# Performance work log

Hardware: AMD Instinct MI355X
Metric: run time of the kernel (lower is better)

The kernel has to match this reference:

```python
import jax, jax.numpy as jnp
import numpy as np

N_NODES = 50000
N_EDGES = 1200000
NODE_DIM = 64
HIDDEN = 64
OUT_DIM = 1
N_LAYERS = 3


def setup_inputs() -> dict:
    key = jax.random.key(0)
    ks = jax.random.split(key, 16)
    inp = {
        "H": jax.random.normal(ks[0], (N_NODES, NODE_DIM), dtype=jnp.float32),
        "edge_index": jax.random.randint(ks[1], (2, N_EDGES), 0, N_NODES, dtype=jnp.int64),
        "E": jax.random.normal(ks[2], (N_EDGES, 16), dtype=jnp.float32),
    }
    # per-layer params: node_encoder (enc) and update_w (upd); weights stored [in, out]
    for i in range(N_LAYERS):
        in_dim = NODE_DIM if i == 0 else HIDDEN
        s = 1.0 / np.sqrt(in_dim)
        inp[f"enc_w{i}"] = jax.random.uniform(ks[3 + 2 * i], (in_dim, HIDDEN), jnp.float32, -s, s)
        inp[f"enc_b{i}"] = jax.random.uniform(ks[4 + 2 * i], (HIDDEN,), jnp.float32, -s, s)
        sh = 1.0 / np.sqrt(HIDDEN)
        inp[f"upd_w{i}"] = jax.random.uniform(ks[9 + 2 * i], (HIDDEN, HIDDEN), jnp.float32, -sh, sh)
        inp[f"upd_b{i}"] = jax.random.uniform(ks[10 + 2 * i], (HIDDEN,), jnp.float32, -sh, sh)
    so = 1.0 / np.sqrt(HIDDEN)
    inp["out_w"] = jax.random.uniform(ks[15], (HIDDEN, OUT_DIM), jnp.float32, -so, so)
    inp["out_b"] = jnp.zeros((OUT_DIM,), jnp.float32)
    return inp


def _gcn_forward(H, edge_index, params):
    u, v = edge_index[0], edge_index[1]
    # symmetric normalization with implicit self-loop degree bump (calc_norm_factor)
    deg = jax.ops.segment_sum(jnp.ones(u.shape[0], H.dtype), u, num_segments=N_NODES) + 1.0
    dis = deg ** -0.5  # deg >= 1, never inf
    norm = dis[u] * dis[v]  # [n_edges]
    for i in range(N_LAYERS):
        enc_w, enc_b, upd_w, upd_b = params[i]
        H = H @ enc_w + enc_b                      # node_encoder
        msgs = norm[:, None] * H[u]                # gather + scale
        agg = jax.ops.segment_sum(msgs, v, num_segments=N_NODES)  # scatter-add
        H = jax.nn.relu((agg + H) @ upd_w + upd_b)  # update + ReLU (dropout = identity in eval)
    return H


def reference(H, edge_index, E, enc_w0, enc_b0, upd_w0, upd_b0, enc_w1, enc_b1,
              upd_w1, upd_b1, enc_w2, enc_b2, upd_w2, upd_b2, out_w, out_b):
    params = [(enc_w0, enc_b0, upd_w0, upd_b0),
              (enc_w1, enc_b1, upd_w1, upd_b1),
              (enc_w2, enc_b2, upd_w2, upd_b2)]
    Hf = _gcn_forward(H, edge_index, params)
    graph_emb = jnp.mean(Hf, axis=0, keepdims=True)  # [1, HIDDEN] readout (batch=None)
    return graph_emb @ out_w + out_b                 # [1, OUT_DIM]
```

## Files before the change

kernel.cpp:

```cpp
#include <hip/hip_runtime.h>
#include <hip/hip_fp16.h>

#define NN 50000
#define NE 1200000
#define DIM 64
#define NB 782
#define SLICES 512
#define ES 2344
#define VCAP 2048
#define GB 782
#define FRONT_LDS 33792


__device__ __forceinline__ void lsort_body(char* smem, const int* __restrict__ ei,
                                           ushort* __restrict__ usort,
                                           int* __restrict__ ebuf,
                                           int* __restrict__ lpart_u,
                                           int* __restrict__ lpart_v,
                                           int s) {
    int* hist = (int*)smem;
    int* wsum = (int*)(smem + 3136);
    ushort* sbu = (ushort*)(smem + 4160);
    int* sbv = (int*)(smem + 8848);
    int t = threadIdx.x;
    int w = t >> 6, l = t & 63;
    int e0 = s * ES, e1 = min(e0 + ES, NE), len = e1 - e0;
    int i0 = t * 4;

    for (int i = t; i < NB; i += 256) hist[i] = 0;
    __syncthreads();
    for (int e = e0 + t; e < e1; e += 256) atomicAdd(&hist[ei[e] >> 6], 1);
    __syncthreads();
    {
        int h0 = (i0 + 0 < NB) ? hist[i0 + 0] : 0;
        int h1 = (i0 + 1 < NB) ? hist[i0 + 1] : 0;
        int h2 = (i0 + 2 < NB) ? hist[i0 + 2] : 0;
        int h3 = (i0 + 3 < NB) ? hist[i0 + 3] : 0;
        int p1 = h0, p2 = h0 + h1, p3 = p2 + h2, p4 = p3 + h3;
        int inc = p4;
        for (int o = 1; o < 64; o <<= 1) {
            int x = __shfl_up(inc, o, 64);
            if (l >= o) inc += x;
        }
        if (l == 63) wsum[w] = inc;
        __syncthreads();
        int base = 0;
#pragma unroll
        for (int j = 0; j < 4; ++j) if (j < w) base += wsum[j];
        int total = wsum[0] + wsum[1] + wsum[2] + wsum[3];
        int excl = base + inc - p4;
        int* lpu = lpart_u + s * (NB + 1);
        if (i0 + 0 < NB) { lpu[i0 + 0] = excl;      hist[i0 + 0] = excl; }
        if (i0 + 1 < NB) { lpu[i0 + 1] = excl + p1; hist[i0 + 1] = excl + p1; }
        if (i0 + 2 < NB) { lpu[i0 + 2] = excl + p2; hist[i0 + 2] = excl + p2; }
        if (i0 + 3 < NB) { lpu[i0 + 3] = excl + p3; hist[i0 + 3] = excl + p3; }
        if (t == 255) lpu[NB] = total;
    }
    __syncthreads();
    for (int e = e0 + t; e < e1; e += 256) {
        int u = ei[e];
        int pos = atomicAdd(&hist[u >> 6], 1);
        sbu[pos] = (ushort)u;
    }
    __syncthreads();
    for (int i = t; i < len; i += 256) usort[e0 + i] = sbu[i];
    for (int i = t; i < NB; i += 256) hist[i] = 0;
    __syncthreads();

    for (int e = e0 + t; e < e1; e += 256) atomicAdd(&hist[ei[NE + e] >> 6], 1);
    __syncthreads();
    {
        int h0 = (i0 + 0 < NB) ? hist[i0 + 0] : 0;
        int h1 = (i0 + 1 < NB) ? hist[i0 + 1] : 0;
        int h2 = (i0 + 2 < NB) ? hist[i0 + 2] : 0;
        int h3 = (i0 + 3 < NB) ? hist[i0 + 3] : 0;
        int p1 = h0, p2 = h0 + h1, p3 = p2 + h2, p4 = p3 + h3;
        int inc = p4;
        for (int o = 1; o < 64; o <<= 1) {
            int x = __shfl_up(inc, o, 64);
            if (l >= o) inc += x;
        }
        if (l == 63) wsum[w] = inc;
        __syncthreads();
        int base = 0;
#pragma unroll
        for (int j = 0; j < 4; ++j) if (j < w) base += wsum[j];
        int total = wsum[0] + wsum[1] + wsum[2] + wsum[3];
        int excl = base + inc - p4;
        int* lpv = lpart_v + s * (NB + 1);
        if (i0 + 0 < NB) { lpv[i0 + 0] = excl;      hist[i0 + 0] = excl; }
        if (i0 + 1 < NB) { lpv[i0 + 1] = excl + p1; hist[i0 + 1] = excl + p1; }
        if (i0 + 2 < NB) { lpv[i0 + 2] = excl + p2; hist[i0 + 2] = excl + p2; }
        if (i0 + 3 < NB) { lpv[i0 + 3] = excl + p3; hist[i0 + 3] = excl + p3; }
        if (t == 255) lpv[NB] = total;
    }
    __syncthreads();
    for (int e = e0 + t; e < e1; e += 256) {
        int u = ei[e], v = ei[NE + e];
        int pos = atomicAdd(&hist[v >> 6], 1);
        sbv[pos] = u | ((v & 63) << 16);
    }
    __syncthreads();
    for (int i = t; i < len; i += 256) ebuf[e0 + i] = sbv[i];
}

__device__ __forceinline__ void gemm_h_body(char* smem, int blk,
                                            const float* __restrict__ A,
                                            const float* __restrict__ W,
                                            const float* __restrict__ bias,
                                            __half* __restrict__ Ch, int M) {
    float (*As)[68] = (float(*)[68])smem;
    float (*Bs)[64] = (float(*)[64])(smem + 17408);
    int t = threadIdx.x;
    int row0 = blk * 64;
#pragma unroll
    for (int i = 0; i < 4; ++i) {
        int idx = t + i * 256;
        int r = idx >> 4, c = (idx & 15) << 2;
        float4 val = make_float4(0.f, 0.f, 0.f, 0.f);
        if (row0 + r < M) val = *(const float4*)&A[(size_t)(row0 + r) * DIM + c];
        *(float4*)&As[r][c] = val;
        *(float4*)&Bs[r][c] = *(const float4*)&W[r * DIM + c];
    }
    __syncthreads();
    int r0 = (t >> 4) * 4;
    int c0 = (t & 15) * 4;
    float acc[4][4] = {};
#pragma unroll
    for (int k = 0; k < 64; k += 4) {
        float4 b0 = *(float4*)&Bs[k + 0][c0];
        float4 b1 = *(float4*)&Bs[k + 1][c0];
        float4 b2 = *(float4*)&Bs[k + 2][c0];
        float4 b3 = *(float4*)&Bs[k + 3][c0];
#pragma unroll
        for (int i = 0; i < 4; ++i) {
            float4 av = *(float4*)&As[r0 + i][k];
            acc[i][0] = fmaf(av.x, b0.x, fmaf(av.y, b1.x, fmaf(av.z, b2.x, fmaf(av.w, b3.x, acc[i][0]))));
            acc[i][1] = fmaf(av.x, b0.y, fmaf(av.y, b1.y, fmaf(av.z, b2.y, fmaf(av.w, b3.y, acc[i][1]))));
            acc[i][2] = fmaf(av.x, b0.z, fmaf(av.y, b1.z, fmaf(av.z, b2.z, fmaf(av.w, b3.z, acc[i][2]))));
            acc[i][3] = fmaf(av.x, b0.w, fmaf(av.y, b1.w, fmaf(av.z, b2.w, fmaf(av.w, b3.w, acc[i][3]))));
        }
    }
    float4 bv = *(const float4*)&bias[c0];
#pragma unroll
    for (int i = 0; i < 4; ++i) {
        int r = row0 + r0 + i;
        if (r < M) {
            __half2 p0 = __floats2half2_rn(acc[i][0] + bv.x, acc[i][1] + bv.y);
            __half2 p1 = __floats2half2_rn(acc[i][2] + bv.z, acc[i][3] + bv.w);
            uint2 pk;
            pk.x = *(unsigned int*)&p0;
            pk.y = *(unsigned int*)&p1;
            *(uint2*)&Ch[(size_t)r * DIM + c0] = pk;
        }
    }
}

__global__ __launch_bounds__(256) void k_front(const int* __restrict__ ei,
                                               ushort* __restrict__ usort,
                                               int* __restrict__ ebuf,
                                               int* __restrict__ lpart_u,
                                               int* __restrict__ lpart_v,
                                               const float* __restrict__ A,
                                               const float* __restrict__ W,
                                               const float* __restrict__ bias,
                                               __half* __restrict__ Ch) {
    extern __shared__ char smem[];
    int b = blockIdx.x;
    if (b < 256)
        lsort_body(smem, ei, usort, ebuf, lpart_u, lpart_v, b);
    else if (b < 512)
        gemm_h_body(smem, b - 256, A, W, bias, Ch, NN);
    else if (b < 768)
        lsort_body(smem, ei, usort, ebuf, lpart_u, lpart_v, b - 256);
    else
        gemm_h_body(smem, b - 512, A, W, bias, Ch, NN);
}

__global__ __launch_bounds__(256) void k_mid(const ushort* __restrict__ usort,
                                             const int* __restrict__ lpart_u,
                                             float* __restrict__ dis,
                                             float* __restrict__ colsum) {
    __shared__ int sh[64];
    int b = blockIdx.x;
    int t = threadIdx.x;
    if (b == 0 && t < 64) colsum[t] = 0.f;
    if (t < 64) sh[t] = 0;
    __syncthreads();
    for (int s = t; s < SLICES; s += 256) {
        const int* row = lpart_u + s * (NB + 1);
        int st = row[b], en = row[b + 1];
        for (int i = st; i < en; ++i)
            atomicAdd(&sh[usort[s * ES + i] & 63], 1);
    }
    __syncthreads();
    int n = (b << 6) + t;
    if (t < 64 && n < NN) dis[n] = rsqrtf((float)sh[t] + 1.0f);
}

__global__ __launch_bounds__(256) void k_vsort(const int* __restrict__ ebuf,
                                               const int* __restrict__ lpart_v,
                                               const float* __restrict__ dis,
                                               int* __restrict__ edges,
                                               int* __restrict__ row_ptr) {
    __shared__ int cache[VCAP];
    __shared__ int cnt[64];
    __shared__ int cur[64];
    __shared__ int wsum[4];
    __shared__ int rsum[4];
    int t = threadIdx.x, w = t >> 6, l = t & 63;
    int b = blockIdx.x;
    int s0 = t * 2, s1 = t * 2 + 1;
    const int* r0p = lpart_v + s0 * (NB + 1);
    const int* r1p = lpart_v + s1 * (NB + 1);
    int a0 = r0p[b], a1 = r0p[b + 1];
    int c0 = r1p[b], c1 = r1p[b + 1];
    int len0 = a1 - a0, len1 = c1 - c0;
    int tl = len0 + len1;
    int ts = a0 + c0;
    int inc = tl;
    for (int o = 1; o < 64; o <<= 1) {
        int x = __shfl_up(inc, o, 64);
        if (l >= o) inc += x;
    }
    int tss = ts;
    for (int off = 32; off; off >>= 1) tss += __shfl_down(tss, off, 64);
    if (l == 63) wsum[w] = inc;
    if (l == 0) rsum[w] = tss;
    if (t < 64) cnt[t] = 0;
    __syncthreads();
    int base = 0;
#pragma unroll
    for (int j = 0; j < 4; ++j) if (j < w) base += wsum[j];
    int n = wsum[0] + wsum[1] + wsum[2] + wsum[3];
    int rbase = rsum[0] + rsum[1] + rsum[2] + rsum[3];
    int pos = base + inc - tl;
    if (n <= VCAP) {
        for (int i = 0; i < len0; ++i) cache[pos + i] = ebuf[s0 * ES + a0 + i];
        int pos1 = pos + len0;
        for (int i = 0; i < len1; ++i) cache[pos1 + i] = ebuf[s1 * ES + c0 + i];
        __syncthreads();
        for (int i = t; i < n; i += 256)
            atomicAdd(&cnt[(cache[i] >> 16) & 63], 1);
        __syncthreads();
        if (w == 0) {
            int c = cnt[l];
            int inc2 = c;
            for (int o = 1; o < 64; o <<= 1) {
                int x = __shfl_up(inc2, o, 64);
                if (l >= o) inc2 += x;
            }
            int excl = inc2 - c;
            cur[l] = rbase + excl;
            row_ptr[(b << 6) + l] = rbase + excl;
        }
        __syncthreads();
        for (int i = t; i < n; i += 256) {
            int rec = cache[i];
            int u = rec & 0xFFFF;
            int p2 = atomicAdd(&cur[(rec >> 16) & 63], 1);
            ushort dh = __half_as_ushort(__float2half_rn(dis[u]));
            edges[p2] = u | ((int)dh << 16);
        }
    } else {
        for (int s = t; s < SLICES; s += 256) {
            const int* row = lpart_v + s * (NB + 1);
            int st = row[b], en = row[b + 1];
            for (int i = st; i < en; ++i)
                atomicAdd(&cnt[(ebuf[s * ES + i] >> 16) & 63], 1);
        }
        __syncthreads();
        if (w == 0) {
            int c = cnt[l];
            int inc2 = c;
            for (int o = 1; o < 64; o <<= 1) {
                int x = __shfl_up(inc2, o, 64);
                if (l >= o) inc2 += x;
            }
            int excl = inc2 - c;
            cur[l] = rbase + excl;
            row_ptr[(b << 6) + l] = rbase + excl;
        }
        __syncthreads();
        for (int s = t; s < SLICES; s += 256) {
            const int* row = lpart_v + s * (NB + 1);
            int st = row[b], en = row[b + 1];
            for (int i = st; i < en; ++i) {
                int rec = ebuf[s * ES + i];
                int u = rec & 0xFFFF;
                int p2 = atomicAdd(&cur[(rec >> 16) & 63], 1);
                ushort dh = __half_as_ushort(__float2half_rn(dis[u]));
                edges[p2] = u | ((int)dh << 16);
            }
        }
    }
}

__global__ __launch_bounds__(256) void k_gemm2(const float* __restrict__ X,
                                               const float* __restrict__ W1,
                                               const float* __restrict__ b1,
                                               const float* __restrict__ W2,
                                               const float* __restrict__ b2,
                                               __half* __restrict__ Zh, int M) {
    __shared__ float As[64][68];
    __shared__ float Bs[64][64];
    int t = threadIdx.x;
    int row0 = blockIdx.x * 64;
#pragma unroll
    for (int i = 0; i < 4; ++i) {
        int idx = t + i * 256;
        int r = idx >> 4, c = (idx & 15) << 2;
        float4 val = make_float4(0.f, 0.f, 0.f, 0.f);
        if (row0 + r < M) val = *(const float4*)&X[(size_t)(row0 + r) * DIM + c];
        *(float4*)&As[r][c] = val;
        *(float4*)&Bs[r][c] = *(const float4*)&W1[r * DIM + c];
    }
    __syncthreads();
    int r0 = (t >> 4) * 4;
    int c0 = (t & 15) * 4;
    float acc[4][4] = {};
#pragma unroll
    for (int k = 0; k < 64; k += 4) {
        float4 v0 = *(float4*)&Bs[k + 0][c0];
        float4 v1 = *(float4*)&Bs[k + 1][c0];
        float4 v2 = *(float4*)&Bs[k + 2][c0];
        float4 v3 = *(float4*)&Bs[k + 3][c0];
#pragma unroll
        for (int i = 0; i < 4; ++i) {
            float4 av = *(float4*)&As[r0 + i][k];
            acc[i][0] = fmaf(av.x, v0.x, fmaf(av.y, v1.x, fmaf(av.z, v2.x, fmaf(av.w, v3.x, acc[i][0]))));
            acc[i][1] = fmaf(av.x, v0.y, fmaf(av.y, v1.y, fmaf(av.z, v2.y, fmaf(av.w, v3.y, acc[i][1]))));
            acc[i][2] = fmaf(av.x, v0.z, fmaf(av.y, v1.z, fmaf(av.z, v2.z, fmaf(av.w, v3.z, acc[i][2]))));
            acc[i][3] = fmaf(av.x, v0.w, fmaf(av.y, v1.w, fmaf(av.z, v2.w, fmaf(av.w, v3.w, acc[i][3]))));
        }
    }
    float4 bv1 = *(const float4*)&b1[c0];
    __syncthreads();
#pragma unroll
    for (int i = 0; i < 4; ++i) {
        float4 y;
        y.x = fmaxf(acc[i][0] + bv1.x, 0.f);
        y.y = fmaxf(acc[i][1] + bv1.y, 0.f);
        y.z = fmaxf(acc[i][2] + bv1.z, 0.f);
        y.w = fmaxf(acc[i][3] + bv1.w, 0.f);
        *(float4*)&As[r0 + i][c0] = y;
    }
#pragma unroll
    for (int i = 0; i < 4; ++i) {
        int idx = t + i * 256;
        int r = idx >> 4, c = (idx & 15) << 2;
        *(float4*)&Bs[r][c] = *(const float4*)&W2[r * DIM + c];
    }
    __syncthreads();
    float acc2[4][4] = {};
#pragma unroll
    for (int k = 0; k < 64; k += 4) {
        float4 v0 = *(float4*)&Bs[k + 0][c0];
        float4 v1 = *(float4*)&Bs[k + 1][c0];
        float4 v2 = *(float4*)&Bs[k + 2][c0];
        float4 v3 = *(float4*)&Bs[k + 3][c0];
#pragma unroll
        for (int i = 0; i < 4; ++i) {
            float4 av = *(float4*)&As[r0 + i][k];
            acc2[i][0] = fmaf(av.x, v0.x, fmaf(av.y, v1.x, fmaf(av.z, v2.x, fmaf(av.w, v3.x, acc2[i][0]))));
            acc2[i][1] = fmaf(av.x, v0.y, fmaf(av.y, v1.y, fmaf(av.z, v2.y, fmaf(av.w, v3.y, acc2[i][1]))));
            acc2[i][2] = fmaf(av.x, v0.z, fmaf(av.y, v1.z, fmaf(av.z, v2.z, fmaf(av.w, v3.z, acc2[i][2]))));
            acc2[i][3] = fmaf(av.x, v0.w, fmaf(av.y, v1.w, fmaf(av.z, v2.w, fmaf(av.w, v3.w, acc2[i][3]))));
        }
    }
    float4 bv2 = *(const float4*)&b2[c0];
#pragma unroll
    for (int i = 0; i < 4; ++i) {
        int r = row0 + r0 + i;
        if (r < M) {
            __half2 p0 = __floats2half2_rn(acc2[i][0] + bv2.x, acc2[i][1] + bv2.y);
            __half2 p1 = __floats2half2_rn(acc2[i][2] + bv2.z, acc2[i][3] + bv2.w);
            uint2 pk;
            pk.x = *(unsigned int*)&p0;
            pk.y = *(unsigned int*)&p1;
            *(uint2*)&Zh[(size_t)r * DIM + c0] = pk;
        }
    }
}

__global__ __launch_bounds__(256) void k_gemm_last(const float* __restrict__ A,
                                                   const float* __restrict__ W,
                                                   const float* __restrict__ bias,
                                                   int M, float* __restrict__ colsum) {
    __shared__ float As[64][68];
    __shared__ float Bs[64][64];
    int t = threadIdx.x;
    int row0 = blockIdx.x * 64;
#pragma unroll
    for (int i = 0; i < 4; ++i) {
        int idx = t + i * 256;
        int r = idx >> 4, c = (idx & 15) << 2;
        float4 val = make_float4(0.f, 0.f, 0.f, 0.f);
        if (row0 + r < M) val = *(const float4*)&A[(size_t)(row0 + r) * DIM + c];
        *(float4*)&As[r][c] = val;
        *(float4*)&Bs[r][c] = *(const float4*)&W[r * DIM + c];
    }
    __syncthreads();
    int r0 = (t >> 4) * 4;
    int c0 = (t & 15) * 4;
    float acc[4][4] = {};
#pragma unroll
    for (int k = 0; k < 64; k += 4) {
        float4 b0 = *(float4*)&Bs[k + 0][c0];
        float4 b1 = *(float4*)&Bs[k + 1][c0];
        float4 b2 = *(float4*)&Bs[k + 2][c0];
        float4 b3 = *(float4*)&Bs[k + 3][c0];
#pragma unroll
        for (int i = 0; i < 4; ++i) {
            float4 av = *(float4*)&As[r0 + i][k];
            acc[i][0] = fmaf(av.x, b0.x, fmaf(av.y, b1.x, fmaf(av.z, b2.x, fmaf(av.w, b3.x, acc[i][0]))));
            acc[i][1] = fmaf(av.x, b0.y, fmaf(av.y, b1.y, fmaf(av.z, b2.y, fmaf(av.w, b3.y, acc[i][1]))));
            acc[i][2] = fmaf(av.x, b0.z, fmaf(av.y, b1.z, fmaf(av.z, b2.z, fmaf(av.w, b3.z, acc[i][2]))));
            acc[i][3] = fmaf(av.x, b0.w, fmaf(av.y, b1.w, fmaf(av.z, b2.w, fmaf(av.w, b3.w, acc[i][3]))));
        }
    }
    float4 bv = *(const float4*)&bias[c0];
    float csum[4] = {0.f, 0.f, 0.f, 0.f};
#pragma unroll
    for (int i = 0; i < 4; ++i) {
        int r = row0 + r0 + i;
        if (r < M) {
            csum[0] += fmaxf(acc[i][0] + bv.x, 0.f);
            csum[1] += fmaxf(acc[i][1] + bv.y, 0.f);
            csum[2] += fmaxf(acc[i][2] + bv.z, 0.f);
            csum[3] += fmaxf(acc[i][3] + bv.w, 0.f);
        }
    }
    float* red = &As[0][0];
    __syncthreads();
    *(float4*)&red[(t >> 4) * 64 + c0] = make_float4(csum[0], csum[1], csum[2], csum[3]);
    __syncthreads();
    if (t < 64) {
        float s = 0.f;
#pragma unroll
        for (int g = 0; g < 16; ++g) s += red[g * 64 + t];
        atomicAdd(&colsum[t], s);
    }
}

__global__ __launch_bounds__(256) void k_agg(const uint4* __restrict__ Hq4,
                                             const float* __restrict__ dis,
                                             const int* __restrict__ row_ptr,
                                             const int* __restrict__ edges,
                                             float* __restrict__ X) {
    __shared__ int se[4][64];
    int w = threadIdx.x >> 6, l = threadIdx.x & 63;
    int node = (blockIdx.x << 2) + w;
    if (node >= NN) return;
    int start = row_ptr[node];
    int num = row_ptr[node + 1] - start;
    int g = l >> 3;
    int p = l & 7;
    float4 a0 = {0.f, 0.f, 0.f, 0.f};
    float4 a1 = {0.f, 0.f, 0.f, 0.f};
    for (int base = 0; base < num; base += 64) {
        int lim = min(64, num - base);
        se[w][l] = (l < lim) ? edges[start + base + l] : 0;
        __builtin_amdgcn_wave_barrier();
        int octs = (lim + 7) >> 3;
        int rr[8]; uint4 hh[8];
#pragma unroll
        for (int q = 0; q < 8; ++q)
            if (q < octs) rr[q] = se[w][8 * q + g];
#pragma unroll
        for (int q = 0; q < 8; ++q)
            if (q < octs) hh[q] = Hq4[((rr[q] & 0xFFFF) << 3) + p];
#pragma unroll
        for (int q = 0; q < 8; ++q)
            if (q < octs) {
                float wt = __half2float(__ushort_as_half((ushort)((unsigned)rr[q] >> 16)));
                float2 f0 = __half22float2(*(const __half2*)&hh[q].x);
                float2 f1 = __half22float2(*(const __half2*)&hh[q].y);
                float2 f2 = __half22float2(*(const __half2*)&hh[q].z);
                float2 f3 = __half22float2(*(const __half2*)&hh[q].w);
                a0.x = fmaf(wt, f0.x, a0.x);
                a0.y = fmaf(wt, f0.y, a0.y);
                a0.z = fmaf(wt, f1.x, a0.z);
                a0.w = fmaf(wt, f1.y, a0.w);
                a1.x = fmaf(wt, f2.x, a1.x);
                a1.y = fmaf(wt, f2.y, a1.y);
                a1.z = fmaf(wt, f3.x, a1.z);
                a1.w = fmaf(wt, f3.y, a1.w);
            }
        __builtin_amdgcn_wave_barrier();
    }
#pragma unroll
    for (int m = 8; m < 64; m <<= 1) {
        a0.x += __shfl_xor(a0.x, m, 64);
        a0.y += __shfl_xor(a0.y, m, 64);
        a0.z += __shfl_xor(a0.z, m, 64);
        a0.w += __shfl_xor(a0.w, m, 64);
        a1.x += __shfl_xor(a1.x, m, 64);
        a1.y += __shfl_xor(a1.y, m, 64);
        a1.z += __shfl_xor(a1.z, m, 64);
        a1.w += __shfl_xor(a1.w, m, 64);
    }
    if (g == 0) {
        uint4 sv = Hq4[(node << 3) + p];
        float2 s0 = __half22float2(*(const __half2*)&sv.x);
        float2 s1 = __half22float2(*(const __half2*)&sv.y);
        float2 s2 = __half22float2(*(const __half2*)&sv.z);
        float2 s3 = __half22float2(*(const __half2*)&sv.w);
        float dv = dis[node];
        float4 o0, o1;
        o0.x = fmaf(dv, a0.x, s0.x);
        o0.y = fmaf(dv, a0.y, s0.y);
        o0.z = fmaf(dv, a0.z, s1.x);
        o0.w = fmaf(dv, a0.w, s1.y);
        o1.x = fmaf(dv, a1.x, s2.x);
        o1.y = fmaf(dv, a1.y, s2.y);
        o1.z = fmaf(dv, a1.z, s3.x);
        o1.w = fmaf(dv, a1.w, s3.y);
        float* xr = &X[((size_t)node << 6) + (p << 3)];
        *(float4*)xr = o0;
        *(float4*)(xr + 4) = o1;
    }
}

__global__ void k_out(const float* __restrict__ colsum, const float* __restrict__ out_w,
                      const float* __restrict__ out_b, float* __restrict__ out) {
    int f = threadIdx.x;
    float v = colsum[f] * (1.0f / (float)NN) * out_w[f];
    for (int off = 32; off; off >>= 1) v += __shfl_down(v, off, 64);
    if (f == 0) out[0] = v + out_b[0];
}

extern "C" void kernel_launch(void* const* d_in, const int* in_sizes, int n_in,
                              void* d_out, int out_size, void* d_ws, size_t ws_size,
                              hipStream_t stream) {
    const float* H  = (const float*)d_in[0];
    const int*   ei = (const int*)d_in[1];
    const float* enc_w[3] = { (const float*)d_in[3], (const float*)d_in[7],  (const float*)d_in[11] };
    const float* enc_b[3] = { (const float*)d_in[4], (const float*)d_in[8],  (const float*)d_in[12] };
    const float* upd_w[3] = { (const float*)d_in[5], (const float*)d_in[9],  (const float*)d_in[13] };
    const float* upd_b[3] = { (const float*)d_in[6], (const float*)d_in[10], (const float*)d_in[14] };
    const float* out_w = (const float*)d_in[15];
    const float* out_b = (const float*)d_in[16];
    float* out = (float*)d_out;

    size_t off = 0;
    auto carve = [&](size_t bytes) {
        void* p = (char*)d_ws + off;
        off = (off + bytes + 255) & ~(size_t)255;
        return p;
    };
    int*    lpart_u = (int*)carve((size_t)SLICES * (NB + 1) * 4);
    int*    lpart_v = (int*)carve((size_t)SLICES * (NB + 1) * 4);
    float*  dis     = (float*)carve((size_t)NN * 4);
    ushort* usort   = (ushort*)carve((size_t)SLICES * ES * 2);
    int*    ebuf    = (int*)carve((size_t)SLICES * ES * 4);
    int*    edges   = (int*)carve((size_t)NE * 4);
    int*    row_ptr = (int*)carve((size_t)(NN + 65) * 4);
    __half* Ch      = (__half*)carve((size_t)NN * DIM * 2);
    float*  X       = (float*)carve((size_t)NN * DIM * 4);
    float*  colsum  = (float*)carve(64 * 4);

    const int AB = (NN + 3) / 4;
    const uint4* Hq4 = (const uint4*)Ch;

    k_front<<<512 + GB, 256, FRONT_LDS, stream>>>(ei, usort, ebuf, lpart_u, lpart_v,
                                                  H, enc_w[0], enc_b[0], Ch);
    k_mid<<<NB, 256, 0, stream>>>(usort, lpart_u, dis, colsum);
    k_vsort<<<NB, 256, 0, stream>>>(ebuf, lpart_v, dis, edges, row_ptr);

    k_agg<<<AB, 256, 0, stream>>>(Hq4, dis, row_ptr, edges, X);
    k_gemm2<<<GB, 256, 0, stream>>>(X, upd_w[0], upd_b[0], enc_w[1], enc_b[1], Ch, NN);
    k_agg<<<AB, 256, 0, stream>>>(Hq4, dis, row_ptr, edges, X);
    k_gemm2<<<GB, 256, 0, stream>>>(X, upd_w[1], upd_b[1], enc_w[2], enc_b[2], Ch, NN);
    k_agg<<<AB, 256, 0, stream>>>(Hq4, dis, row_ptr, edges, X);
    k_gemm_last<<<GB, 256, 0, stream>>>(X, upd_w[2], upd_b[2], NN, colsum);

    k_out<<<1, 64, 0, stream>>>(colsum, out_w, out_b, out);
}
```

Measured before the change: 374.6 us.

## Merge degree and v-sort kernels, store aggregates in fp16, compact edge list

Several changes at once. The degree/dis kernel and the v-sort kernel are merged into one launch, and the v-sort no longer reads dis, so the two halves can run concurrently. Edges become 16-bit source ids, with the dis weight now gathered inside the aggregation kernel. The aggregation output X is stored as fp16, halving its write and read traffic. The local sort keeps edge indices in registers instead of reloading them, and the front kernel gets an occupancy hint. The cost is an extra dependent gather of dis per edge in k_agg and lower precision in the intermediate aggregate.

```diff
diff --git a/kernel.cpp b/kernel.cpp
--- a/kernel.cpp
+++ b/kernel.cpp
@@ -27,9 +27,19 @@
     int e0 = s * ES, e1 = min(e0 + ES, NE), len = e1 - e0;
     int i0 = t * 4;
 
+    int uv[10], vv[10];
+#pragma unroll
+    for (int j = 0; j < 10; ++j) {
+        int e = e0 + t + j * 256;
+        uv[j] = (e < e1) ? ei[e] : -1;
+        vv[j] = (e < e1) ? ei[NE + e] : -1;
+    }
+
     for (int i = t; i < NB; i += 256) hist[i] = 0;
     __syncthreads();
-    for (int e = e0 + t; e < e1; e += 256) atomicAdd(&hist[ei[e] >> 6], 1);
+#pragma unroll
+    for (int j = 0; j < 10; ++j)
+        if (uv[j] >= 0) atomicAdd(&hist[uv[j] >> 6], 1);
     __syncthreads();
     {
         int h0 = (i0 + 0 < NB) ? hist[i0 + 0] : 0;
@@ -57,17 +67,20 @@
         if (t == 255) lpu[NB] = total;
     }
     __syncthreads();
-    for (int e = e0 + t; e < e1; e += 256) {
-        int u = ei[e];
-        int pos = atomicAdd(&hist[u >> 6], 1);
-        sbu[pos] = (ushort)u;
-    }
+#pragma unroll
+    for (int j = 0; j < 10; ++j)
+        if (uv[j] >= 0) {
+            int pos = atomicAdd(&hist[uv[j] >> 6], 1);
+            sbu[pos] = (ushort)uv[j];
+        }
     __syncthreads();
     for (int i = t; i < len; i += 256) usort[e0 + i] = sbu[i];
     for (int i = t; i < NB; i += 256) hist[i] = 0;
     __syncthreads();
 
-    for (int e = e0 + t; e < e1; e += 256) atomicAdd(&hist[ei[NE + e] >> 6], 1);
+#pragma unroll
+    for (int j = 0; j < 10; ++j)
+        if (vv[j] >= 0) atomicAdd(&hist[vv[j] >> 6], 1);
     __syncthreads();
     {
         int h0 = (i0 + 0 < NB) ? hist[i0 + 0] : 0;
@@ -95,11 +108,12 @@
         if (t == 255) lpv[NB] = total;
     }
     __syncthreads();
-    for (int e = e0 + t; e < e1; e += 256) {
-        int u = ei[e], v = ei[NE + e];
-        int pos = atomicAdd(&hist[v >> 6], 1);
-        sbv[pos] = u | ((v & 63) << 16);
-    }
+#pragma unroll
+    for (int j = 0; j < 10; ++j)
+        if (vv[j] >= 0) {
+            int pos = atomicAdd(&hist[vv[j] >> 6], 1);
+            sbv[pos] = uv[j] | ((vv[j] & 63) << 16);
+        }
     __syncthreads();
     for (int i = t; i < len; i += 256) ebuf[e0 + i] = sbv[i];
 }
@@ -156,15 +170,15 @@
     }
 }
 
-__global__ __launch_bounds__(256) void k_front(const int* __restrict__ ei,
-                                               ushort* __restrict__ usort,
-                                               int* __restrict__ ebuf,
-                                               int* __restrict__ lpart_u,
-                                               int* __restrict__ lpart_v,
-                                               const float* __restrict__ A,
-                                               const float* __restrict__ W,
-                                               const float* __restrict__ bias,
-                                               __half* __restrict__ Ch) {
+__global__ __launch_bounds__(256, 2) void k_front(const int* __restrict__ ei,
+                                                  ushort* __restrict__ usort,
+                                                  int* __restrict__ ebuf,
+                                                  int* __restrict__ lpart_u,
+                                                  int* __restrict__ lpart_v,
+                                                  const float* __restrict__ A,
+                                                  const float* __restrict__ W,
+                                                  const float* __restrict__ bias,
+                                                  __half* __restrict__ Ch) {
     extern __shared__ char smem[];
     int b = blockIdx.x;
     if (b < 256)
@@ -177,39 +191,39 @@
         gemm_h_body(smem, b - 512, A, W, bias, Ch, NN);
 }
 
-__global__ __launch_bounds__(256) void k_mid(const ushort* __restrict__ usort,
-                                             const int* __restrict__ lpart_u,
-                                             float* __restrict__ dis,
-                                             float* __restrict__ colsum) {
-    __shared__ int sh[64];
-    int b = blockIdx.x;
-    int t = threadIdx.x;
-    if (b == 0 && t < 64) colsum[t] = 0.f;
-    if (t < 64) sh[t] = 0;
-    __syncthreads();
-    for (int s = t; s < SLICES; s += 256) {
-        const int* row = lpart_u + s * (NB + 1);
-        int st = row[b], en = row[b + 1];
-        for (int i = st; i < en; ++i)
-            atomicAdd(&sh[usort[s * ES + i] & 63], 1);
-    }
-    __syncthreads();
-    int n = (b << 6) + t;
-    if (t < 64 && n < NN) dis[n] = rsqrtf((float)sh[t] + 1.0f);
-}
-
-__global__ __launch_bounds__(256) void k_vsort(const int* __restrict__ ebuf,
-                                               const int* __restrict__ lpart_v,
-                                               const float* __restrict__ dis,
-                                               int* __restrict__ edges,
-                                               int* __restrict__ row_ptr) {
+__global__ __launch_bounds__(256) void k_prep(const ushort* __restrict__ usort,
+                                              const int* __restrict__ lpart_u,
+                                              const int* __restrict__ ebuf,
+                                              const int* __restrict__ lpart_v,
+                                              float* __restrict__ dis,
+                                              ushort* __restrict__ edges,
+                                              int* __restrict__ row_ptr,
+                                              float* __restrict__ colsum) {
     __shared__ int cache[VCAP];
     __shared__ int cnt[64];
     __shared__ int cur[64];
-    __shared__ int wsum[4];
-    __shared__ int rsum[4];
+    __shared__ int wsum4[4];
+    __shared__ int rsum4[4];
+    __shared__ int sh[64];
+    int bid = blockIdx.x;
     int t = threadIdx.x, w = t >> 6, l = t & 63;
-    int b = blockIdx.x;
+    if (bid < NB) {
+        int b = bid;
+        if (b == 0 && t < 64) colsum[t] = 0.f;
+        if (t < 64) sh[t] = 0;
+        __syncthreads();
+        for (int s = t; s < SLICES; s += 256) {
+            const int* row = lpart_u + s * (NB + 1);
+            int st = row[b], en = row[b + 1];
+            for (int i = st; i < en; ++i)
+                atomicAdd(&sh[usort[s * ES + i] & 63], 1);
+        }
+        __syncthreads();
+        int n = (b << 6) + t;
+        if (t < 64 && n < NN) dis[n] = rsqrtf((float)sh[t] + 1.0f);
+        return;
+    }
+    int b = bid - NB;
     int s0 = t * 2, s1 = t * 2 + 1;
     const int* r0p = lpart_v + s0 * (NB + 1);
     const int* r1p = lpart_v + s1 * (NB + 1);
@@ -225,15 +239,15 @@
     }
     int tss = ts;
     for (int off = 32; off; off >>= 1) tss += __shfl_down(tss, off, 64);
-    if (l == 63) wsum[w] = inc;
-    if (l == 0) rsum[w] = tss;
+    if (l == 63) wsum4[w] = inc;
+    if (l == 0) rsum4[w] = tss;
     if (t < 64) cnt[t] = 0;
     __syncthreads();
     int base = 0;
 #pragma unroll
-    for (int j = 0; j < 4; ++j) if (j < w) base += wsum[j];
-    int n = wsum[0] + wsum[1] + wsum[2] + wsum[3];
-    int rbase = rsum[0] + rsum[1] + rsum[2] + rsum[3];
+    for (int j = 0; j < 4; ++j) if (j < w) base += wsum4[j];
+    int n = wsum4[0] + wsum4[1] + wsum4[2] + wsum4[3];
+    int rbase = rsum4[0] + rsum4[1] + rsum4[2] + rsum4[3];
     int pos = base + inc - tl;
     if (n <= VCAP) {
         for (int i = 0; i < len0; ++i) cache[pos + i] = ebuf[s0 * ES + a0 + i];
@@ -257,10 +271,8 @@
         __syncthreads();
         for (int i = t; i < n; i += 256) {
             int rec = cache[i];
-            int u = rec & 0xFFFF;
             int p2 = atomicAdd(&cur[(rec >> 16) & 63], 1);
-            ushort dh = __half_as_ushort(__float2half_rn(dis[u]));
-            edges[p2] = u | ((int)dh << 16);
+            edges[p2] = (ushort)(rec & 0xFFFF);
         }
     } else {
         for (int s = t; s < SLICES; s += 256) {
@@ -287,16 +299,14 @@
             int st = row[b], en = row[b + 1];
             for (int i = st; i < en; ++i) {
                 int rec = ebuf[s * ES + i];
-                int u = rec & 0xFFFF;
                 int p2 = atomicAdd(&cur[(rec >> 16) & 63], 1);
-                ushort dh = __half_as_ushort(__float2half_rn(dis[u]));
-                edges[p2] = u | ((int)dh << 16);
+                edges[p2] = (ushort)(rec & 0xFFFF);
             }
         }
     }
 }
 
-__global__ __launch_bounds__(256) void k_gemm2(const float* __restrict__ X,
+__global__ __launch_bounds__(256) void k_gemm2(const __half* __restrict__ Xh,
                                                const float* __restrict__ W1,
                                                const float* __restrict__ b1,
                                                const float* __restrict__ W2,
@@ -311,7 +321,12 @@
         int idx = t + i * 256;
         int r = idx >> 4, c = (idx & 15) << 2;
         float4 val = make_float4(0.f, 0.f, 0.f, 0.f);
-        if (row0 + r < M) val = *(const float4*)&X[(size_t)(row0 + r) * DIM + c];
+        if (row0 + r < M) {
+            uint2 hv = *(const uint2*)&Xh[(size_t)(row0 + r) * DIM + c];
+            float2 f0 = __half22float2(*(const __half2*)&hv.x);
+            float2 f1 = __half22float2(*(const __half2*)&hv.y);
+            val = make_float4(f0.x, f0.y, f1.x, f1.y);
+        }
         *(float4*)&As[r][c] = val;
         *(float4*)&Bs[r][c] = *(const float4*)&W1[r * DIM + c];
     }
@@ -383,7 +398,7 @@
     }
 }
 
-__global__ __launch_bounds__(256) void k_gemm_last(const float* __restrict__ A,
+__global__ __launch_bounds__(256) void k_gemm_last(const __half* __restrict__ Xh,
                                                    const float* __restrict__ W,
                                                    const float* __restrict__ bias,
                                                    int M, float* __restrict__ colsum) {
@@ -396,7 +411,12 @@
         int idx = t + i * 256;
         int r = idx >> 4, c = (idx & 15) << 2;
         float4 val = make_float4(0.f, 0.f, 0.f, 0.f);
-        if (row0 + r < M) val = *(const float4*)&A[(size_t)(row0 + r) * DIM + c];
+        if (row0 + r < M) {
+            uint2 hv = *(const uint2*)&Xh[(size_t)(row0 + r) * DIM + c];
+            float2 f0 = __half22float2(*(const __half2*)&hv.x);
+            float2 f1 = __half22float2(*(const __half2*)&hv.y);
+            val = make_float4(f0.x, f0.y, f1.x, f1.y);
+        }
         *(float4*)&As[r][c] = val;
         *(float4*)&Bs[r][c] = *(const float4*)&W[r * DIM + c];
     }
@@ -446,9 +466,10 @@
 __global__ __launch_bounds__(256) void k_agg(const uint4* __restrict__ Hq4,
                                              const float* __restrict__ dis,
                                              const int* __restrict__ row_ptr,
-                                             const int* __restrict__ edges,
-                                             float* __restrict__ X) {
-    __shared__ int se[4][64];
+                                             const ushort* __restrict__ edges,
+                                             __half* __restrict__ Xh) {
+    __shared__ ushort se[4][64];
+    __shared__ float swt[4][64];
     int w = threadIdx.x >> 6, l = threadIdx.x & 63;
     int node = (blockIdx.x << 2) + w;
     if (node >= NN) return;
@@ -460,20 +481,24 @@
     float4 a1 = {0.f, 0.f, 0.f, 0.f};
     for (int base = 0; base < num; base += 64) {
         int lim = min(64, num - base);
-        se[w][l] = (l < lim) ? edges[start + base + l] : 0;
+        ushort u = 0;
+        float wv = 0.f;
+        if (l < lim) { u = edges[start + base + l]; wv = dis[u]; }
+        se[w][l] = u;
+        swt[w][l] = wv;
         __builtin_amdgcn_wave_barrier();
         int octs = (lim + 7) >> 3;
-        int rr[8]; uint4 hh[8];
+        int rr[8]; float ww[8]; uint4 hh[8];
 #pragma unroll
         for (int q = 0; q < 8; ++q)
-            if (q < octs) rr[q] = se[w][8 * q + g];
+            if (q < octs) { rr[q] = se[w][8 * q + g]; ww[q] = swt[w][8 * q + g]; }
 #pragma unroll
         for (int q = 0; q < 8; ++q)
-            if (q < octs) hh[q] = Hq4[((rr[q] & 0xFFFF) << 3) + p];
+            if (q < octs) hh[q] = Hq4[(rr[q] << 3) + p];
 #pragma unroll
         for (int q = 0; q < 8; ++q)
             if (q < octs) {
-                float wt = __half2float(__ushort_as_half((ushort)((unsigned)rr[q] >> 16)));
+                float wt = ww[q];
                 float2 f0 = __half22float2(*(const __half2*)&hh[q].x);
                 float2 f1 = __half22float2(*(const __half2*)&hh[q].y);
                 float2 f2 = __half22float2(*(const __half2*)&hh[q].z);
@@ -507,18 +532,16 @@
         float2 s2 = __half22float2(*(const __half2*)&sv.z);
         float2 s3 = __half22float2(*(const __half2*)&sv.w);
         float dv = dis[node];
-        float4 o0, o1;
-        o0.x = fmaf(dv, a0.x, s0.x);
-        o0.y = fmaf(dv, a0.y, s0.y);
-        o0.z = fmaf(dv, a0.z, s1.x);
-        o0.w = fmaf(dv, a0.w, s1.y);
-        o1.x = fmaf(dv, a1.x, s2.x);
-        o1.y = fmaf(dv, a1.y, s2.y);
-        o1.z = fmaf(dv, a1.z, s3.x);
-        o1.w = fmaf(dv, a1.w, s3.y);
-        float* xr = &X[((size_t)node << 6) + (p << 3)];
-        *(float4*)xr = o0;
-        *(float4*)(xr + 4) = o1;
+        __half2 h0 = __floats2half2_rn(fmaf(dv, a0.x, s0.x), fmaf(dv, a0.y, s0.y));
+        __half2 h1 = __floats2half2_rn(fmaf(dv, a0.z, s1.x), fmaf(dv, a0.w, s1.y));
+        __half2 h2 = __floats2half2_rn(fmaf(dv, a1.x, s2.x), fmaf(dv, a1.y, s2.y));
+        __half2 h3 = __floats2half2_rn(fmaf(dv, a1.z, s3.x), fmaf(dv, a1.w, s3.y));
+        uint4 pk;
+        pk.x = *(unsigned int*)&h0;
+        pk.y = *(unsigned int*)&h1;
+        pk.z = *(unsigned int*)&h2;
+        pk.w = *(unsigned int*)&h3;
+        *(uint4*)&Xh[((size_t)node << 6) + (p << 3)] = pk;
     }
 }
 
@@ -554,10 +577,10 @@
     float*  dis     = (float*)carve((size_t)NN * 4);
     ushort* usort   = (ushort*)carve((size_t)SLICES * ES * 2);
     int*    ebuf    = (int*)carve((size_t)SLICES * ES * 4);
-    int*    edges   = (int*)carve((size_t)NE * 4);
+    ushort* edges   = (ushort*)carve((size_t)NE * 2);
     int*    row_ptr = (int*)carve((size_t)(NN + 65) * 4);
     __half* Ch      = (__half*)carve((size_t)NN * DIM * 2);
-    float*  X       = (float*)carve((size_t)NN * DIM * 4);
+    __half* Xh      = (__half*)carve((size_t)NN * DIM * 2);
     float*  colsum  = (float*)carve(64 * 4);
 
     const int AB = (NN + 3) / 4;
@@ -565,15 +588,15 @@
 
     k_front<<<512 + GB, 256, FRONT_LDS, stream>>>(ei, usort, ebuf, lpart_u, lpart_v,
                                                   H, enc_w[0], enc_b[0], Ch);
-    k_mid<<<NB, 256, 0, stream>>>(usort, lpart_u, dis, colsum);
-    k_vsort<<<NB, 256, 0, stream>>>(ebuf, lpart_v, dis, edges, row_ptr);
-
-    k_agg<<<AB, 256, 0, stream>>>(Hq4, dis, row_ptr, edges, X);
-    k_gemm2<<<GB, 256, 0, stream>>>(X, upd_w[0], upd_b[0], enc_w[1], enc_b[1], Ch, NN);
-    k_agg<<<AB, 256, 0, stream>>>(Hq4, dis, row_ptr, edges, X);
-    k_gemm2<<<GB, 256, 0, stream>>>(X, upd_w[1], upd_b[1], enc_w[2], enc_b[2], Ch, NN);
-    k_agg<<<AB, 256, 0, stream>>>(Hq4, dis, row_ptr, edges, X);
-    k_gemm_last<<<GB, 256, 0, stream>>>(X, upd_w[2], upd_b[2], NN, colsum);
+    k_prep<<<2 * NB, 256, 0, stream>>>(usort, lpart_u, ebuf, lpart_v,
+                                       dis, edges, row_ptr, colsum);
+
+    k_agg<<<AB, 256, 0, stream>>>(Hq4, dis, row_ptr, edges, Xh);
+    k_gemm2<<<GB, 256, 0, stream>>>(Xh, upd_w[0], upd_b[0], enc_w[1], enc_b[1], Ch, NN);
+    k_agg<<<AB, 256, 0, stream>>>(Hq4, dis, row_ptr, edges, Xh);
+    k_gemm2<<<GB, 256, 0, stream>>>(Xh, upd_w[1], upd_b[1], enc_w[2], enc_b[2], Ch, NN);
+    k_agg<<<AB, 256, 0, stream>>>(Hq4, dis, row_ptr, edges, Xh);
+    k_gemm_last<<<GB, 256, 0, stream>>>(Xh, upd_w[2], upd_b[2], NN, colsum);
 
     k_out<<<1, 64, 0, stream>>>(colsum, out_w, out_b, out);
 }
```

Measured after the change: 377.0 us. No clear change (+0.7%).
